# Performance work log

Hardware: AMD Instinct MI355X
Metric: run time of the kernel (lower is better)

Reference implementation:

```python
import jax, jax.numpy as jnp
import numpy as np

B, P, N, C = 8, 4, 512, 768
H = 12
HD = C // H  # 64
SCALE = HD ** -0.5


def setup_inputs() -> dict:
    key = jax.random.key(0)
    k1, k2, k3 = jax.random.split(key, 3)
    x = jax.random.normal(k1, (B, P, N, C), dtype=jnp.float32)
    W_qkv = jax.random.normal(k2, (3 * C, C), dtype=jnp.float32) * (C ** -0.5)
    W_proj = jax.random.normal(k3, (C, C), dtype=jnp.float32) * (C ** -0.5)
    b_proj = jnp.zeros((C,), dtype=jnp.float32)
    return {"x": x, "W_qkv": W_qkv, "W_proj": W_proj, "b_proj": b_proj}


def reference(x, W_qkv, W_proj, b_proj):
    b, p, n, c = x.shape
    # qkv projection (no bias): (B,P,N,3C) -> (B,P,N,3,H,HD)
    qkv = jnp.einsum('bpnc,dc->bpnd', x, W_qkv).reshape(b, p, n, 3, H, HD)
    # -> (3, B, P, H, N, HD)
    qkv = jnp.transpose(qkv, (3, 0, 1, 4, 2, 5))
    q, k, v = qkv[0], qkv[1], qkv[2]
    # scaled dot-product attention per (batch, patch, head)
    attn = jnp.einsum('bphnd,bphmd->bphnm', q * SCALE, k)
    attn = jax.nn.softmax(attn, axis=-1)
    out = jnp.einsum('bphnm,bphmd->bphnd', attn, v)
    # merge heads: (B,P,N,H,HD) -> (B,P,N,C)
    out = jnp.transpose(out, (0, 1, 3, 2, 4)).reshape(b, p, n, c)
    return jnp.einsum('bpnc,dc->bpnd', out, W_proj) + b_proj
```

## Files before the change

### kernel.cpp

```cpp
#include <hip/hip_runtime.h>

typedef __bf16 bf16x8 __attribute__((ext_vector_type(8)));
typedef unsigned short u16x8 __attribute__((ext_vector_type(8)));
typedef short s16x4 __attribute__((ext_vector_type(4)));
typedef unsigned short u16x4 __attribute__((ext_vector_type(4)));
typedef float f32x4 __attribute__((ext_vector_type(4)));

#define GLOAD_LDS16(GP, LP)                                                        \
  __builtin_amdgcn_global_load_lds((const __attribute__((address_space(1))) void*)(GP), \
                                   (__attribute__((address_space(3))) void*)(LP), 16, 0, 0)

__device__ __forceinline__ unsigned short f2bf(float f) {
  unsigned int u = __builtin_bit_cast(unsigned int, f);
  u += 0x7FFFu + ((u >> 16) & 1u);
  return (unsigned short)(u >> 16);
}
__device__ __forceinline__ bf16x8 ldfrag(const unsigned short* p) {
  return __builtin_bit_cast(bf16x8, *(const u16x8*)p);
}
__device__ __forceinline__ s16x4 ldfrag4(const unsigned short* p) {
  return __builtin_bit_cast(s16x4, *(const u16x4*)p);
}
__device__ __forceinline__ f32x4 mfma16(bf16x8 a, bf16x8 b, f32x4 c) {
  return __builtin_amdgcn_mfma_f32_16x16x32_bf16(a, b, c, 0, 0, 0);
}
__device__ __forceinline__ f32x4 mfma1k(s16x4 a, s16x4 b, f32x4 c) {
  return __builtin_amdgcn_mfma_f32_16x16x16bf16_1k(a, b, c, 0, 0, 0);
}

#define MTOK   16384
#define CDIM   768
#define C3     2304
#define C2     1536
#define NX     12582912
#define NQW    1769472
#define NPW    589824

#define QSCALE_LOG2E 0.1803368801111204f

#define XB_OFF    0ul
#define WQKV_OFF  25165824ul
#define WPROJ_OFF 28704768ul
#define QK_OFF    29884416ul
#define VT_OFF    80216064ul

__global__ __launch_bounds__(256) void convert_kernel(
    const float* __restrict__ x, const float* __restrict__ wqkv,
    const float* __restrict__ wproj, unsigned short* __restrict__ xb,
    unsigned short* __restrict__ wqkvb, unsigned short* __restrict__ wprojb) {
  const int NX4 = NX / 4, NQ4 = NQW / 4, NP4 = NPW / 4;
  const int total = NX4 + NQ4 + NP4;
  for (int i = blockIdx.x * 256 + threadIdx.x; i < total; i += gridDim.x * 256) {
    const float4* src; unsigned short* dst; float scale = 1.f; int j;
    if (i < NX4) { src = (const float4*)x; dst = xb; j = i; }
    else if (i < NX4 + NQ4) {
      j = i - NX4; src = (const float4*)wqkv; dst = wqkvb;
      int d = (j * 4) / CDIM; if (d < CDIM) scale = QSCALE_LOG2E;
    } else { j = i - NX4 - NQ4; src = (const float4*)wproj; dst = wprojb; }
    float4 v = src[j];
    unsigned int lo = f2bf(v.x * scale) | ((unsigned)f2bf(v.y * scale) << 16);
    unsigned int hi = f2bf(v.z * scale) | ((unsigned)f2bf(v.w * scale) << 16);
    uint2 pk; pk.x = lo; pk.y = hi;
    *(uint2*)(dst + (long)j * 4) = pk;
  }
}

template <int MODE>
__global__ __launch_bounds__(256) void gemm_bt(
    const unsigned short* __restrict__ A, const unsigned short* __restrict__ B,
    int K, int Nout,
    unsigned short* __restrict__ out_qk, unsigned short* __restrict__ out_vT,
    float* __restrict__ out_f32, const float* __restrict__ bias) {
  __shared__ unsigned short As[128 * 32];
  __shared__ unsigned short Bs[128 * 32];
  const int tid = threadIdx.x;
  const int wave = tid >> 6, lane = tid & 63;
  const int wy = wave >> 1, wx = wave & 1;
  const int l15 = lane & 15, quad = lane >> 4;
  const int bm = blockIdx.x, bn = blockIdx.y;

  f32x4 acc[4][4];
  for (int i = 0; i < 4; i++)
    for (int j = 0; j < 4; j++) acc[i][j] = f32x4{0.f, 0.f, 0.f, 0.f};

  const long Abase = (long)bm * 128 * K;
  const long Bbase = (long)bn * 128 * K;

  for (int kk = 0; kk < K; kk += 32) {
    for (int i = 0; i < 2; i++) {
      int c = wave * 128 + i * 64 + lane;
      int row = c >> 2, c16 = c & 3;
      GLOAD_LDS16(A + Abase + (long)row * K + kk + c16 * 8, As + c * 8);
      GLOAD_LDS16(B + Bbase + (long)row * K + kk + c16 * 8, Bs + c * 8);
    }
    __syncthreads();
    bf16x8 af[4], bfr[4];
    for (int mt = 0; mt < 4; mt++) af[mt]  = ldfrag(As + (wy * 64 + mt * 16 + l15) * 32 + quad * 8);
    for (int nt = 0; nt < 4; nt++) bfr[nt] = ldfrag(Bs + (wx * 64 + nt * 16 + l15) * 32 + quad * 8);
    for (int mt = 0; mt < 4; mt++)
      for (int nt = 0; nt < 4; nt++)
        acc[mt][nt] = mfma16(af[mt], bfr[nt], acc[mt][nt]);
    __syncthreads();
  }

  if (MODE == 0) {
    if (bn < 12) {
      for (int mt = 0; mt < 4; mt++) {
        int mg = bm * 128 + wy * 64 + mt * 16 + quad * 4;
        for (int nt = 0; nt < 4; nt++) {
          int d = bn * 128 + wx * 64 + nt * 16 + l15;
          for (int r = 0; r < 4; r++)
            out_qk[(long)(mg + r) * C2 + d] = f2bf(acc[mt][nt][r]);
        }
      }
    } else {
      for (int mt = 0; mt < 4; mt++) {
        int mg = bm * 128 + wy * 64 + mt * 16 + quad * 4;
        int bp = mg >> 9, n0 = mg & 511;
        for (int nt = 0; nt < 4; nt++) {
          int dp = bn * 128 - C2 + wx * 64 + nt * 16 + l15;
          int hh = dp >> 6, e = dp & 63;
          unsigned int lo = f2bf(acc[mt][nt][0]) | ((unsigned)f2bf(acc[mt][nt][1]) << 16);
          unsigned int hi = f2bf(acc[mt][nt][2]) | ((unsigned)f2bf(acc[mt][nt][3]) << 16);
          uint2 pk; pk.x = lo; pk.y = hi;
          *(uint2*)(out_vT + ((long)((bp * 12 + hh) * 64 + e) * 512 + n0)) = pk;
        }
      }
    }
  } else {
    for (int nt = 0; nt < 4; nt++) {
      int d = bn * 128 + wx * 64 + nt * 16 + l15;
      float bv = bias[d];
      for (int mt = 0; mt < 4; mt++) {
        int mg = bm * 128 + wy * 64 + mt * 16 + quad * 4;
        for (int r = 0; r < 4; r++)
          out_f32[(long)(mg + r) * Nout + d] = acc[mt][nt][r] + bv;
      }
    }
  }
}

__global__ __launch_bounds__(256, 4) void attn_kernel(
    const unsigned short* __restrict__ qk, const unsigned short* __restrict__ vT,
    unsigned short* __restrict__ aout) {
  const int bph = blockIdx.x;
  const int qt  = blockIdx.y;
  const int bp = bph / 12, h = bph % 12;
  const int tid = threadIdx.x;
  const int wave = tid >> 6, lane = tid & 63;
  const int l15 = lane & 15, quad = lane >> 4;

  __shared__ unsigned short Qs[128 * 72];
  __shared__ unsigned short Ks[64 * 72];
  __shared__ unsigned short Vs[64 * 72];

  const unsigned short* Qg = qk + (long)(bp * 512 + qt * 128) * C2 + h * 64;
  const unsigned short* Kg = qk + (long)(bp * 512) * C2 + CDIM + h * 64;
  const unsigned short* Vg = vT + (long)(bp * 12 + h) * 64 * 512;

  for (int i = 0; i < 4; i++) {
    int c = tid + i * 256;
    int row = c >> 3, c8 = c & 7;
    *(uint4*)(Qs + row * 72 + c8 * 8) = *(const uint4*)(Qg + (long)row * C2 + c8 * 8);
  }

  f32x4 o[2][4];
  float mrow[2], lrow[2];
  for (int a = 0; a < 2; a++) {
    for (int b = 0; b < 4; b++) o[a][b] = f32x4{0.f, 0.f, 0.f, 0.f};
    mrow[a] = -1e30f; lrow[a] = 0.f;
  }

  for (int ch = 0; ch < 8; ch++) {
    if (ch) __syncthreads();
    for (int i = 0; i < 2; i++) {
      int c = tid + i * 256;
      int row = c >> 3, c8 = c & 7;
      *(uint4*)(Ks + row * 72 + c8 * 8) = *(const uint4*)(Kg + (long)(ch * 64 + row) * C2 + c8 * 8);
      *(uint4*)(Vs + row * 72 + c8 * 8) = *(const uint4*)(Vg + (long)row * 512 + ch * 64 + c8 * 8);
    }
    __syncthreads();

    f32x4 st[2][4];
    for (int a = 0; a < 2; a++)
      for (int b = 0; b < 4; b++) st[a][b] = f32x4{0.f, 0.f, 0.f, 0.f};
    for (int ks = 0; ks < 2; ks++) {
      bf16x8 qf[2];
      qf[0] = ldfrag(Qs + (wave * 32 +      l15) * 72 + ks * 32 + quad * 8);
      qf[1] = ldfrag(Qs + (wave * 32 + 16 + l15) * 72 + ks * 32 + quad * 8);
      for (int nt = 0; nt < 4; nt++) {
        bf16x8 kf = ldfrag(Ks + (nt * 16 + l15) * 72 + ks * 32 + quad * 8);
        st[0][nt] = mfma16(kf, qf[0], st[0][nt]);
        st[1][nt] = mfma16(kf, qf[1], st[1][nt]);
      }
    }

    s16x4 pf[2][4];
    for (int mt2 = 0; mt2 < 2; mt2++) {
      float mx = -1e30f;
      for (int nt = 0; nt < 4; nt++)
        for (int r = 0; r < 4; r++) mx = fmaxf(mx, st[mt2][nt][r]);
      mx = fmaxf(mx, __shfl_xor(mx, 16));
      mx = fmaxf(mx, __shfl_xor(mx, 32));
      float mnew = fmaxf(mrow[mt2], mx);
      float alpha = __builtin_amdgcn_exp2f(mrow[mt2] - mnew);
      mrow[mt2] = mnew;
      float rs = 0.f;
      for (int nt = 0; nt < 4; nt++) {
        f32x4 p;
        for (int r = 0; r < 4; r++) {
          p[r] = __builtin_amdgcn_exp2f(st[mt2][nt][r] - mnew);
          rs += p[r];
        }
        s16x4 pk;
        for (int r = 0; r < 4; r++) pk[r] = (short)f2bf(p[r]);
        pf[mt2][nt] = pk;
      }
      rs += __shfl_xor(rs, 16);
      rs += __shfl_xor(rs, 32);
      lrow[mt2] = lrow[mt2] * alpha + rs;
      for (int et = 0; et < 4; et++) o[mt2][et] *= alpha;
    }

    for (int nt = 0; nt < 4; nt++)
      for (int et = 0; et < 4; et++) {
        s16x4 vf = ldfrag4(Vs + (et * 16 + l15) * 72 + nt * 16 + quad * 4);
        o[0][et] = mfma1k(vf, pf[0][nt], o[0][et]);
        o[1][et] = mfma1k(vf, pf[1][nt], o[1][et]);
      }
  }

  for (int mt2 = 0; mt2 < 2; mt2++) {
    float inv = 1.f / lrow[mt2];
    int q = qt * 128 + wave * 32 + mt2 * 16 + l15;
    for (int et = 0; et < 4; et++) {
      unsigned int lo = f2bf(o[mt2][et][0] * inv) | ((unsigned)f2bf(o[mt2][et][1] * inv) << 16);
      unsigned int hi = f2bf(o[mt2][et][2] * inv) | ((unsigned)f2bf(o[mt2][et][3] * inv) << 16);
      uint2 pk; pk.x = lo; pk.y = hi;
      *(uint2*)(aout + (long)(bp * 512 + q) * CDIM + h * 64 + et * 16 + quad * 4) = pk;
    }
  }
}

extern "C" void kernel_launch(void* const* d_in, const int* in_sizes, int n_in,
                              void* d_out, int out_size, void* d_ws, size_t ws_size,
                              hipStream_t stream) {
  (void)in_sizes; (void)n_in; (void)out_size; (void)ws_size;
  const float* x     = (const float*)d_in[0];
  const float* wqkv  = (const float*)d_in[1];
  const float* wproj = (const float*)d_in[2];
  const float* bproj = (const float*)d_in[3];
  float* out = (float*)d_out;
  char* ws = (char*)d_ws;

  unsigned short* xb     = (unsigned short*)(ws + XB_OFF);
  unsigned short* wqkvb  = (unsigned short*)(ws + WQKV_OFF);
  unsigned short* wprojb = (unsigned short*)(ws + WPROJ_OFF);
  unsigned short* qkbuf  = (unsigned short*)(ws + QK_OFF);
  unsigned short* vTbuf  = (unsigned short*)(ws + VT_OFF);
  unsigned short* attn_o = xb;

  convert_kernel<<<2048, 256, 0, stream>>>(x, wqkv, wproj, xb, wqkvb, wprojb);
  gemm_bt<0><<<dim3(128, 18), 256, 0, stream>>>(xb, wqkvb, CDIM, C3, qkbuf, vTbuf, nullptr, nullptr);
  attn_kernel<<<dim3(384, 4), 256, 0, stream>>>(qkbuf, vTbuf, attn_o);
  gemm_bt<1><<<dim3(128, 6), 256, 0, stream>>>(attn_o, wprojb, CDIM, CDIM, nullptr, nullptr, out, bproj);
}
```

Measured before the change: 279.2 us.

## Use BK=64 XOR-swizzled LDS tiles and operand-swapped MFMA for vectorized GEMM stores

Doubles the GEMM K-tile to 64 with an XOR swizzle on LDS rows, which halves the barrier count and avoids bank conflicts. For the QK and output-projection GEMMs it swaps the MFMA operands so each lane holds four consecutive columns, which allows packed 8-byte bf16 and float4 f32 stores instead of scalar ones. The QKV GEMM is split into separate Q/K and V launches so each launch has a single epilogue path. K is now hardcoded to 768, and the extra launch adds a little overhead.

```diff
diff --git a/kernel.cpp b/kernel.cpp
--- a/kernel.cpp
+++ b/kernel.cpp
@@ -68,11 +68,12 @@
 template <int MODE>
 __global__ __launch_bounds__(256) void gemm_bt(
     const unsigned short* __restrict__ A, const unsigned short* __restrict__ B,
-    int K, int Nout,
-    unsigned short* __restrict__ out_qk, unsigned short* __restrict__ out_vT,
-    float* __restrict__ out_f32, const float* __restrict__ bias) {
-  __shared__ unsigned short As[128 * 32];
-  __shared__ unsigned short Bs[128 * 32];
+    unsigned short* __restrict__ out_bf, float* __restrict__ out_f32,
+    const float* __restrict__ bias) {
+  constexpr int K = 768;
+  constexpr bool SWAP = (MODE != 1);
+  __shared__ unsigned short As[128 * 64];
+  __shared__ unsigned short Bs[128 * 64];
   const int tid = threadIdx.x;
   const int wave = tid >> 6, lane = tid & 63;
   const int wy = wave >> 1, wx = wave & 1;
@@ -86,55 +87,71 @@
   const long Abase = (long)bm * 128 * K;
   const long Bbase = (long)bn * 128 * K;
 
-  for (int kk = 0; kk < K; kk += 32) {
-    for (int i = 0; i < 2; i++) {
-      int c = wave * 128 + i * 64 + lane;
-      int row = c >> 2, c16 = c & 3;
-      GLOAD_LDS16(A + Abase + (long)row * K + kk + c16 * 8, As + c * 8);
-      GLOAD_LDS16(B + Bbase + (long)row * K + kk + c16 * 8, Bs + c * 8);
+  long goff[4]; int ldsoff[4];
+  for (int i = 0; i < 4; i++) {
+    int c = wave * 256 + i * 64 + lane;
+    int row = c >> 3, q = c & 7;
+    int srcq = q ^ (row & 7);
+    goff[i] = (long)row * K + srcq * 8;
+    ldsoff[i] = c * 8;
+  }
+  const int slot0 = (quad ^ (l15 & 7)) * 8;
+  const int slot1 = ((4 + quad) ^ (l15 & 7)) * 8;
+
+  for (int kk = 0; kk < K; kk += 64) {
+    for (int i = 0; i < 4; i++) {
+      GLOAD_LDS16(A + Abase + goff[i] + kk, As + ldsoff[i]);
+      GLOAD_LDS16(B + Bbase + goff[i] + kk, Bs + ldsoff[i]);
     }
     __syncthreads();
-    bf16x8 af[4], bfr[4];
-    for (int mt = 0; mt < 4; mt++) af[mt]  = ldfrag(As + (wy * 64 + mt * 16 + l15) * 32 + quad * 8);
-    for (int nt = 0; nt < 4; nt++) bfr[nt] = ldfrag(Bs + (wx * 64 + nt * 16 + l15) * 32 + quad * 8);
-    for (int mt = 0; mt < 4; mt++)
-      for (int nt = 0; nt < 4; nt++)
-        acc[mt][nt] = mfma16(af[mt], bfr[nt], acc[mt][nt]);
+    for (int ks = 0; ks < 2; ks++) {
+      const int sl = ks ? slot1 : slot0;
+      bf16x8 af[4], bfr[4];
+      for (int mt = 0; mt < 4; mt++) af[mt]  = ldfrag(As + (wy * 64 + mt * 16 + l15) * 64 + sl);
+      for (int nt = 0; nt < 4; nt++) bfr[nt] = ldfrag(Bs + (wx * 64 + nt * 16 + l15) * 64 + sl);
+      for (int mt = 0; mt < 4; mt++)
+        for (int nt = 0; nt < 4; nt++) {
+          if (SWAP) acc[mt][nt] = mfma16(bfr[nt], af[mt], acc[mt][nt]);
+          else      acc[mt][nt] = mfma16(af[mt], bfr[nt], acc[mt][nt]);
+        }
+    }
     __syncthreads();
   }
 
   if (MODE == 0) {
-    if (bn < 12) {
-      for (int mt = 0; mt < 4; mt++) {
-        int mg = bm * 128 + wy * 64 + mt * 16 + quad * 4;
-        for (int nt = 0; nt < 4; nt++) {
-          int d = bn * 128 + wx * 64 + nt * 16 + l15;
-          for (int r = 0; r < 4; r++)
-            out_qk[(long)(mg + r) * C2 + d] = f2bf(acc[mt][nt][r]);
-        }
-      }
-    } else {
-      for (int mt = 0; mt < 4; mt++) {
-        int mg = bm * 128 + wy * 64 + mt * 16 + quad * 4;
-        int bp = mg >> 9, n0 = mg & 511;
-        for (int nt = 0; nt < 4; nt++) {
-          int dp = bn * 128 - C2 + wx * 64 + nt * 16 + l15;
-          int hh = dp >> 6, e = dp & 63;
-          unsigned int lo = f2bf(acc[mt][nt][0]) | ((unsigned)f2bf(acc[mt][nt][1]) << 16);
-          unsigned int hi = f2bf(acc[mt][nt][2]) | ((unsigned)f2bf(acc[mt][nt][3]) << 16);
-          uint2 pk; pk.x = lo; pk.y = hi;
-          *(uint2*)(out_vT + ((long)((bp * 12 + hh) * 64 + e) * 512 + n0)) = pk;
-        }
+    for (int mt = 0; mt < 4; mt++) {
+      int m = bm * 128 + wy * 64 + mt * 16 + l15;
+      for (int nt = 0; nt < 4; nt++) {
+        int d0 = bn * 128 + wx * 64 + nt * 16 + quad * 4;
+        unsigned int lo = f2bf(acc[mt][nt][0]) | ((unsigned)f2bf(acc[mt][nt][1]) << 16);
+        unsigned int hi = f2bf(acc[mt][nt][2]) | ((unsigned)f2bf(acc[mt][nt][3]) << 16);
+        uint2 pk; pk.x = lo; pk.y = hi;
+        *(uint2*)(out_bf + (long)m * C2 + d0) = pk;
+      }
+    }
+  } else if (MODE == 1) {
+    for (int mt = 0; mt < 4; mt++) {
+      int mg = bm * 128 + wy * 64 + mt * 16 + quad * 4;
+      int bp = mg >> 9, n0 = mg & 511;
+      for (int nt = 0; nt < 4; nt++) {
+        int dp = bn * 128 + wx * 64 + nt * 16 + l15;
+        int hh = dp >> 6, e = dp & 63;
+        unsigned int lo = f2bf(acc[mt][nt][0]) | ((unsigned)f2bf(acc[mt][nt][1]) << 16);
+        unsigned int hi = f2bf(acc[mt][nt][2]) | ((unsigned)f2bf(acc[mt][nt][3]) << 16);
+        uint2 pk; pk.x = lo; pk.y = hi;
+        *(uint2*)(out_bf + ((long)((bp * 12 + hh) * 64 + e) * 512 + n0)) = pk;
       }
     }
   } else {
     for (int nt = 0; nt < 4; nt++) {
-      int d = bn * 128 + wx * 64 + nt * 16 + l15;
-      float bv = bias[d];
+      int d0 = bn * 128 + wx * 64 + nt * 16 + quad * 4;
+      float4 bv = *(const float4*)(bias + d0);
       for (int mt = 0; mt < 4; mt++) {
-        int mg = bm * 128 + wy * 64 + mt * 16 + quad * 4;
-        for (int r = 0; r < 4; r++)
-          out_f32[(long)(mg + r) * Nout + d] = acc[mt][nt][r] + bv;
+        int m = bm * 128 + wy * 64 + mt * 16 + l15;
+        float4 o;
+        o.x = acc[mt][nt][0] + bv.x; o.y = acc[mt][nt][1] + bv.y;
+        o.z = acc[mt][nt][2] + bv.z; o.w = acc[mt][nt][3] + bv.w;
+        *(float4*)(out_f32 + (long)m * CDIM + d0) = o;
       }
     }
   }
@@ -261,7 +278,8 @@
   unsigned short* attn_o = xb;
 
   convert_kernel<<<2048, 256, 0, stream>>>(x, wqkv, wproj, xb, wqkvb, wprojb);
-  gemm_bt<0><<<dim3(128, 18), 256, 0, stream>>>(xb, wqkvb, CDIM, C3, qkbuf, vTbuf, nullptr, nullptr);
+  gemm_bt<0><<<dim3(128, 12), 256, 0, stream>>>(xb, wqkvb, qkbuf, nullptr, nullptr);
+  gemm_bt<1><<<dim3(128, 6), 256, 0, stream>>>(xb, wqkvb + (long)C2 * CDIM, vTbuf, nullptr, nullptr);
   attn_kernel<<<dim3(384, 4), 256, 0, stream>>>(qkbuf, vTbuf, attn_o);
-  gemm_bt<1><<<dim3(128, 6), 256, 0, stream>>>(attn_o, wprojb, CDIM, CDIM, nullptr, nullptr, out, bproj);
-}
+  gemm_bt<2><<<dim3(128, 6), 256, 0, stream>>>(attn_o, wprojb, nullptr, out, bproj);
+}
```

New measurement: 267.9 us. -4.0%, faster.
